# Performance work log

Measured on AMD Instinct MI355X. Metric: run time of the kernel, lower is better.

Reference implementation:

```python
import jax, jax.numpy as jnp
import numpy as np

EMBED_DIM = 1024
NUM_HEADS = 16
HEAD_DIM = EMBED_DIM // NUM_HEADS
MASKED = True


def setup_inputs() -> dict:
    key = jax.random.key(0)
    ks = jax.random.split(key, 9)
    B, S, E = 4, 2048, EMBED_DIM
    sc = 1.0 / np.sqrt(E)
    return {
        "x": jax.random.normal(ks[0], (B, S, E), jnp.float32),
        "wq": jax.random.normal(ks[1], (E, E), jnp.float32) * sc,
        "bq": jax.random.normal(ks[2], (E,), jnp.float32) * 0.02,
        "wk": jax.random.normal(ks[3], (E, E), jnp.float32) * sc,
        "bk": jax.random.normal(ks[4], (E,), jnp.float32) * 0.02,
        "wv": jax.random.normal(ks[5], (E, E), jnp.float32) * sc,
        "bv": jax.random.normal(ks[6], (E,), jnp.float32) * 0.02,
        "wo": jax.random.normal(ks[7], (E, E), jnp.float32) * sc,
        "bo": jax.random.normal(ks[8], (E,), jnp.float32) * 0.02,
    }


def reference(x, wq, bq, wk, bk, wv, bv, wo, bo):
    B, S, E = x.shape
    H, Dh = NUM_HEADS, HEAD_DIM
    # QKV projections, then split heads: [B,S,E] -> [B,H,S,Dh]
    def split(t):
        return t.reshape(B, S, H, Dh).transpose(0, 2, 1, 3)
    q = split(x @ wq.T + bq)
    k = split(x @ wk.T + bk)
    v = split(x @ wv.T + bv)
    scale = Dh ** 0.5
    scores = jnp.einsum('bhsd,bhtd->bhst', q, k) / scale  # [B,H,S,S]
    if MASKED:
        causal = jnp.tril(jnp.ones((S, S), dtype=bool))
        scores = jnp.where(causal, scores, -jnp.inf)
    weights = jax.nn.softmax(scores, axis=-1)
    ctx = jnp.einsum('bhst,bhtd->bhsd', weights, v)
    ctx = ctx.transpose(0, 2, 1, 3).reshape(B, S, E)
    return ctx @ wo.T + bo
```

## Files before the change

kernel.cpp:

```cpp
#include <hip/hip_runtime.h>
#include <hip/hip_bf16.h>

#define EMB   1024
#define SEQ   2048
#define BATCH 4
#define NH    16
#define DHEAD 64
#define MROWS (BATCH*SEQ)
#define NSTRIP (SEQ/32)
#define QSCALE 0.18033688011112042f

typedef float f32x4  __attribute__((ext_vector_type(4)));
typedef float f32x16 __attribute__((ext_vector_type(16)));
typedef short s16x8  __attribute__((ext_vector_type(8)));

__device__ __forceinline__ f32x4 mfma16(s16x8 a, s16x8 b, f32x4 c) {
    return __builtin_amdgcn_mfma_f32_16x16x32_bf16(a, b, c, 0, 0, 0);
}
__device__ __forceinline__ f32x16 mfma32(s16x8 a, s16x8 b, f32x16 c) {
    return __builtin_amdgcn_mfma_f32_32x32x16_bf16(a, b, c, 0, 0, 0);
}

__device__ __forceinline__ unsigned short f2bf(float f) {
    __hip_bfloat16 h = __float2bfloat16(f);
    return __builtin_bit_cast(unsigned short, h);
}

__device__ __forceinline__ unsigned cvtpk(float lo, float hi) {
    unsigned r;
    asm("v_cvt_pk_bf16_f32 %0, %1, %2" : "=v"(r) : "v"(lo), "v"(hi));
    return r;
}

__device__ __forceinline__ void plane_swap(unsigned &a, unsigned &b) {
    asm("v_permlane32_swap_b32 %0, %1" : "+v"(a), "+v"(b));
}

__device__ __forceinline__ s16x8 frag4(unsigned a, unsigned b, unsigned c, unsigned d) {
    union { unsigned u[4]; s16x8 f; } x;
    x.u[0] = a; x.u[1] = b; x.u[2] = c; x.u[3] = d;
    return x.f;
}

__device__ __forceinline__ float exp2r(float x) {
    float r;
    asm("v_exp_f32 %0, %1" : "=v"(r) : "v"(x));
    return r;
}
__device__ __forceinline__ float max3f(float a, float b, float c) {
    float r;
    asm("v_max3_f32 %0, %1, %2, %3" : "=v"(r) : "v"(a), "v"(b), "v"(c));
    return r;
}

__global__ void cvt_all(const float* __restrict__ x,
                        const float* __restrict__ w0, const float* __restrict__ w1,
                        const float* __restrict__ w2, const float* __restrict__ w3,
                        unsigned short* __restrict__ xb,
                        unsigned short* __restrict__ o0, unsigned short* __restrict__ o1,
                        unsigned short* __restrict__ o2, unsigned short* __restrict__ o3,
                        int nx4, int nw4) {
    int i = blockIdx.x * blockDim.x + threadIdx.x;
    const float* in; unsigned short* out; int n;
    switch (blockIdx.y) {
        case 0:  in = x;  out = xb; n = nx4; break;
        case 1:  in = w0; out = o0; n = nw4; break;
        case 2:  in = w1; out = o1; n = nw4; break;
        case 3:  in = w2; out = o2; n = nw4; break;
        default: in = w3; out = o3; n = nw4; break;
    }
    if (i >= n) return;
    float4 v = reinterpret_cast<const float4*>(in)[i];
    ushort4 o;
    o.x = f2bf(v.x); o.y = f2bf(v.y); o.z = f2bf(v.z); o.w = f2bf(v.w);
    reinterpret_cast<ushort4*>(out)[i] = o;
}

#define GLDS(g, s) __builtin_amdgcn_global_load_lds((const __attribute__((address_space(1))) void*)(g), \
                       (__attribute__((address_space(3))) void*)(s), 16, 0, 0)

__global__ __launch_bounds__(256) void gemm_qkv(const unsigned short* __restrict__ A,
                                                const unsigned short* __restrict__ wqb,
                                                const unsigned short* __restrict__ wkb,
                                                const unsigned short* __restrict__ wvb,
                                                const float* __restrict__ bq,
                                                const float* __restrict__ bk,
                                                const float* __restrict__ bv,
                                                unsigned short* __restrict__ qB,
                                                unsigned short* __restrict__ kB,
                                                unsigned short* __restrict__ vtB) {
    __shared__ unsigned short sA0[128*32];
    __shared__ unsigned short sB0[128*32];
    __shared__ unsigned short sA1[128*32];
    __shared__ unsigned short sB1[128*32];
    const int tid = threadIdx.x;
    const int w  = tid >> 6, l = tid & 63;
    const int lg = l >> 4,  lr = l & 15;
    const int nb  = blockIdx.x;
    const int seg = nb >> 3;
    const int mBase = blockIdx.y * 128;
    const int nBase = (nb & 7) * 128;
    const unsigned short* Bw = (seg == 0) ? wqb : (seg == 1) ? wkb : wvb;
    const float* bias = (seg == 0) ? bq : (seg == 1) ? bk : bv;
    const int wr = w >> 1, wc = w & 1;
    const int srow = l >> 2;
    const int sk0  = (l & 3) * 8;
    const bool segV = (seg == 2);

    f32x4 acc[4][4] = {};

    auto STAGE = [&](unsigned short* dA, unsigned short* dB, int kb) {
        #pragma unroll
        for (int rr = 0; rr < 2; ++rr) {
            const int chunk = w + rr * 4;
            const unsigned short* ga = A  + (size_t)(mBase + chunk*16 + srow) * EMB + kb + sk0;
            GLDS(ga, &dA[chunk * 512]);
            const unsigned short* gb = Bw + (size_t)(nBase + chunk*16 + srow) * EMB + kb + sk0;
            GLDS(gb, &dB[chunk * 512]);
        }
    };
    auto COMPUTE = [&](const unsigned short* dA, const unsigned short* dB) {
        s16x8 af[4], bf[4];
        #pragma unroll
        for (int mi = 0; mi < 4; ++mi)
            af[mi] = *reinterpret_cast<const s16x8*>(&dA[(wr*64 + mi*16 + lr)*32 + lg*8]);
        #pragma unroll
        for (int ni = 0; ni < 4; ++ni)
            bf[ni] = *reinterpret_cast<const s16x8*>(&dB[(wc*64 + ni*16 + lr)*32 + lg*8]);
        if (segV) {
            #pragma unroll
            for (int mi = 0; mi < 4; ++mi)
                #pragma unroll
                for (int ni = 0; ni < 4; ++ni)
                    acc[ni][mi] = mfma16(bf[ni], af[mi], acc[ni][mi]);
        } else {
            #pragma unroll
            for (int mi = 0; mi < 4; ++mi)
                #pragma unroll
                for (int ni = 0; ni < 4; ++ni)
                    acc[mi][ni] = mfma16(af[mi], bf[ni], acc[mi][ni]);
        }
    };

    STAGE(sA0, sB0, 0);
    __syncthreads();
    for (int kb = 0; kb < EMB; kb += 64) {
        STAGE(sA1, sB1, kb + 32);
        COMPUTE(sA0, sB0);
        __syncthreads();
        if (kb + 64 < EMB) STAGE(sA0, sB0, kb + 64);
        COMPUTE(sA1, sB1);
        __syncthreads();
    }

    const int colBase = nBase + wc * 64;
    const int rowBase = mBase + wr * 64;
    if (!segV) {
        unsigned short* outp = seg ? kB : qB;
        const float oscale = seg ? 1.0f : QSCALE;
        #pragma unroll
        for (int ni = 0; ni < 4; ++ni) {
            const int col = colBase + ni*16 + lr;
            const float bv = bias[col];
            const int h = col >> 6, d = col & 63;
            const int inner = ((d >> 4) * 2 + ((d >> 3) & 1)) * 256 + (d & 7);
            #pragma unroll
            for (int mi = 0; mi < 4; ++mi) {
                #pragma unroll
                for (int r = 0; r < 4; ++r) {
                    const int gr = rowBase + mi*16 + lg*4 + r;
                    const int b = gr >> 11, sin_ = gr & 2047;
                    const int strip = sin_ >> 5, l31q = sin_ & 31;
                    outp[(size_t)(b*NH + h) * (SEQ*DHEAD) + strip*2048 + inner + l31q*8]
                        = f2bf((acc[mi][ni][r] + bv) * oscale);
                }
            }
        }
    } else {
        #pragma unroll
        for (int ni = 0; ni < 4; ++ni) {
            #pragma unroll
            for (int r = 0; r < 4; ++r) {
                const int n = colBase + ni*16 + lg*4 + r;
                const float bv = bias[n];
                const int h = n >> 6, d = n & 63;
                #pragma unroll
                for (int mi = 0; mi < 4; ++mi) {
                    const int tok = rowBase + mi*16 + lr;
                    const int b = tok >> 11, sv = tok & 2047;
                    const int kvt = sv >> 5, ks = (sv >> 4) & 1, hi2 = (sv >> 3) & 1, j = sv & 7;
                    vtB[(size_t)(b*NH + h) * (SEQ*DHEAD) + kvt*2048 + (ks*2 + hi2)*512 + d*8 + j]
                        = f2bf(acc[ni][mi][r] + bv);
                }
            }
        }
    }
}

__global__ __launch_bounds__(256) void gemm_out(const unsigned short* __restrict__ A,
                                                const unsigned short* __restrict__ Bw,
                                                const float* __restrict__ bias,
                                                float* __restrict__ Out) {
    __shared__ unsigned short sA0[128*32];
    __shared__ unsigned short sB0[128*32];
    __shared__ unsigned short sA1[128*32];
    __shared__ unsigned short sB1[128*32];
    const int tid = threadIdx.x;
    const int w  = tid >> 6, l = tid & 63;
    const int lg = l >> 4,  lr = l & 15;
    const int mBase = blockIdx.y * 128;
    const int nBase = blockIdx.x * 128;
    const int wr = w >> 1, wc = w & 1;
    const int srow = l >> 2;
    const int sk0  = (l & 3) * 8;

    f32x4 acc[4][4] = {};

    auto STAGE = [&](unsigned short* dA, unsigned short* dB, int kb) {
        #pragma unroll
        for (int rr = 0; rr < 2; ++rr) {
            const int chunk = w + rr * 4;
            const unsigned short* ga = A  + (size_t)(mBase + chunk*16 + srow) * EMB + kb + sk0;
            GLDS(ga, &dA[chunk * 512]);
            const unsigned short* gb = Bw + (size_t)(nBase + chunk*16 + srow) * EMB + kb + sk0;
            GLDS(gb, &dB[chunk * 512]);
        }
    };
    auto COMPUTE = [&](const unsigned short* dA, const unsigned short* dB) {
        s16x8 af[4], bf[4];
        #pragma unroll
        for (int mi = 0; mi < 4; ++mi)
            af[mi] = *reinterpret_cast<const s16x8*>(&dA[(wr*64 + mi*16 + lr)*32 + lg*8]);
        #pragma unroll
        for (int ni = 0; ni < 4; ++ni)
            bf[ni] = *reinterpret_cast<const s16x8*>(&dB[(wc*64 + ni*16 + lr)*32 + lg*8]);
        #pragma unroll
        for (int mi = 0; mi < 4; ++mi)
            #pragma unroll
            for (int ni = 0; ni < 4; ++ni)
                acc[mi][ni] = mfma16(af[mi], bf[ni], acc[mi][ni]);
    };

    STAGE(sA0, sB0, 0);
    __syncthreads();
    for (int kb = 0; kb < EMB; kb += 64) {
        STAGE(sA1, sB1, kb + 32);
        COMPUTE(sA0, sB0);
        __syncthreads();
        if (kb + 64 < EMB) STAGE(sA0, sB0, kb + 64);
        COMPUTE(sA1, sB1);
        __syncthreads();
    }

    const int colBase = nBase + wc * 64;
    const int rowBase = mBase + wr * 64;
    #pragma unroll
    for (int ni = 0; ni < 4; ++ni) {
        const int col = colBase + ni*16 + lr;
        const float bv = bias[col];
        #pragma unroll
        for (int mi = 0; mi < 4; ++mi) {
            #pragma unroll
            for (int r = 0; r < 4; ++r) {
                const int gr = rowBase + mi*16 + lg*4 + r;
                Out[(size_t)gr * EMB + col] = acc[mi][ni][r] + bv;
            }
        }
    }
}

__global__ __launch_bounds__(128) void attn_fwd(const unsigned short* __restrict__ qb,
                                                const unsigned short* __restrict__ kb,
                                                const unsigned short* __restrict__ vb,
                                                unsigned short* __restrict__ ctx) {
    __shared__ __align__(16) unsigned sld[2][32*36];
    const int tid = threadIdx.x;
    const int wv_ = tid >> 6;
    const int l = tid & 63;
    const int l31 = l & 31, hi = l >> 5;
    const int bh = blockIdx.x & 63;
    const int pair = (int)blockIdx.x >> 6;
    const int strip = wv_ ? (NSTRIP - 1 - pair) : pair;
    const int q0 = strip * 32;
    const size_t hbase = (size_t)bh * SEQ * DHEAD;
    const unsigned short* qh = qb + hbase;
    const unsigned short* kh = kb + hbase;
    const unsigned short* vh = vb + hbase;

    s16x8 qf[4];
    #pragma unroll
    for (int s = 0; s < 4; ++s)
        qf[s] = *reinterpret_cast<const s16x8*>(&qh[strip*2048 + s*512 + l*8]);

    f32x16 o0 = {}, o1 = {};
    float m = -__builtin_inff(), lsum = 0.f;
    const int ntiles = strip + 1;

    s16x8 kfA[4], vfA[4], kfB[4], vfB[4];

    auto LOADKV = [&](s16x8* kf, s16x8* vf, int t) {
        const unsigned short* kp = kh + t*2048;
        #pragma unroll
        for (int s = 0; s < 4; ++s)
            kf[s] = *reinterpret_cast<const s16x8*>(&kp[s*512 + l*8]);
        const unsigned short* vp = vh + t*2048 + hi*512 + l31*8;
        #pragma unroll
        for (int ks = 0; ks < 2; ++ks) {
            vf[ks]     = *reinterpret_cast<const s16x8*>(&vp[ks*1024]);
            vf[2 + ks] = *reinterpret_cast<const s16x8*>(&vp[ks*1024 + 256]);
        }
    };

    auto BODY = [&](s16x8* kf, s16x8* vf, int t) {
        f32x16 sa = {};
        #pragma unroll
        for (int s = 0; s < 4; ++s) sa = mfma32(kf[s], qf[s], sa);

        if (t == strip) {
            #pragma unroll
            for (int r = 0; r < 16; ++r) {
                const int kvloc = (r & 3) + 8*(r >> 2) + 4*hi;
                if (kvloc > l31) sa[r] = -__builtin_inff();
            }
        }

        const float a0 = max3f(sa[0],  sa[1],  sa[2]);
        const float a1 = max3f(sa[3],  sa[4],  sa[5]);
        const float a2 = max3f(sa[6],  sa[7],  sa[8]);
        const float a3 = max3f(sa[9],  sa[10], sa[11]);
        const float a4 = max3f(sa[12], sa[13], sa[14]);
        const float b0 = max3f(a0, a1, a2);
        const float b1 = max3f(a3, a4, sa[15]);
        float pm = fmaxf(b0, b1);
        pm = fmaxf(pm, __shfl_xor(pm, 32));

        float mn = m;
        if (!__all(pm <= m + 8.0f)) {
            mn = fmaxf(m, pm);
            const float fs = exp2r(m - mn);
            o0 *= fs; o1 *= fs; lsum *= fs;
            m = mn;
        }

        #pragma unroll
        for (int r = 0; r < 16; ++r) sa[r] = exp2r(sa[r] - mn);

        const float s0 = sa[0]+sa[1],   s1 = sa[2]+sa[3],   s2 = sa[4]+sa[5],   s3 = sa[6]+sa[7];
        const float s4 = sa[8]+sa[9],   s5 = sa[10]+sa[11], s6 = sa[12]+sa[13], s7 = sa[14]+sa[15];
        const float t0 = s0+s1, t1 = s2+s3, t2 = s4+s5, t3 = s6+s7;
        float rs = (t0+t1) + (t2+t3);
        rs += __shfl_xor(rs, 32);
        lsum += rs;

        unsigned u[4], v[4];
        #pragma unroll
        for (int r2 = 0; r2 < 4; ++r2) {
            u[r2] = cvtpk(sa[4*r2 + 0], sa[4*r2 + 1]);
            v[r2] = cvtpk(sa[4*r2 + 2], sa[4*r2 + 3]);
        }
        plane_swap(u[0], u[1]); plane_swap(v[0], v[1]);
        plane_swap(u[2], u[3]); plane_swap(v[2], v[3]);
        const s16x8 pf0 = frag4(u[0], v[0], u[1], v[1]);
        const s16x8 pf1 = frag4(u[2], v[2], u[3], v[3]);

        o0 = mfma32(vf[0], pf0, o0);
        o0 = mfma32(vf[1], pf1, o0);
        o1 = mfma32(vf[2], pf0, o1);
        o1 = mfma32(vf[3], pf1, o1);
    };

    LOADKV(kfA, vfA, 0);
    int t = 0;
    for (; t + 1 < ntiles; t += 2) {
        LOADKV(kfB, vfB, t + 1);
        BODY(kfA, vfA, t);
        if (t + 2 < ntiles) LOADKV(kfA, vfA, t + 2);
        BODY(kfB, vfB, t + 1);
    }
    if (t < ntiles) BODY(kfA, vfA, t);

    const float inv = 1.0f / lsum;
    unsigned* my = sld[wv_];
    #pragma unroll
    for (int dt = 0; dt < 2; ++dt) {
        #pragma unroll
        for (int r2 = 0; r2 < 4; ++r2) {
            const float e0 = (dt ? o1[4*r2+0] : o0[4*r2+0]) * inv;
            const float e1 = (dt ? o1[4*r2+1] : o0[4*r2+1]) * inv;
            const float e2 = (dt ? o1[4*r2+2] : o0[4*r2+2]) * inv;
            const float e3 = (dt ? o1[4*r2+3] : o0[4*r2+3]) * inv;
            const int col = 4*r2 + 2*hi + 16*dt;
            my[l31*36 + col]     = cvtpk(e0, e1);
            my[l31*36 + col + 1] = cvtpk(e2, e3);
        }
    }
    asm volatile("s_waitcnt lgkmcnt(0)" ::: "memory");
    __builtin_amdgcn_sched_barrier(0);
    const int row = l >> 1, half = l & 1;
    const unsigned* rp = &my[row*36 + half*16];
    const int b = bh >> 4, h = bh & 15;
    unsigned short* op = &ctx[((size_t)b*SEQ + q0 + row) * EMB + h*DHEAD + half*32];
    #pragma unroll
    for (int i = 0; i < 4; ++i) {
        uint4 d4 = *reinterpret_cast<const uint4*>(rp + i*4);
        *reinterpret_cast<uint4*>(op + i*8) = d4;
    }
}

extern "C" void kernel_launch(void* const* d_in, const int* in_sizes, int n_in,
                              void* d_out, int out_size, void* d_ws, size_t ws_size,
                              hipStream_t stream) {
    const float* x  = (const float*)d_in[0];
    const float* wq = (const float*)d_in[1];
    const float* bq = (const float*)d_in[2];
    const float* wk = (const float*)d_in[3];
    const float* bk = (const float*)d_in[4];
    const float* wv = (const float*)d_in[5];
    const float* bv = (const float*)d_in[6];
    const float* wo = (const float*)d_in[7];
    const float* bo = (const float*)d_in[8];
    float* out = (float*)d_out;

    char* ws = (char*)d_ws;
    const size_t MB = 1ull << 20;
    unsigned short* xb  = (unsigned short*)(ws);
    unsigned short* wqb = (unsigned short*)(ws + 16*MB);
    unsigned short* wkb = (unsigned short*)(ws + 18*MB);
    unsigned short* wvb = (unsigned short*)(ws + 20*MB);
    unsigned short* wob = (unsigned short*)(ws + 22*MB);
    unsigned short* qB  = (unsigned short*)(ws + 24*MB);
    unsigned short* kB  = (unsigned short*)(ws + 40*MB);
    unsigned short* vtB = (unsigned short*)(ws + 56*MB);
    unsigned short* ctx = xb;

    const int nx4 = MROWS * EMB / 4;
    const int nw4 = EMB * EMB / 4;
    cvt_all<<<dim3((nx4 + 255)/256, 5), 256, 0, stream>>>(x, wq, wk, wv, wo,
                                                          xb, wqb, wkb, wvb, wob, nx4, nw4);

    gemm_qkv<<<dim3(24, MROWS/128), 256, 0, stream>>>(xb, wqb, wkb, wvb, bq, bk, bv, qB, kB, vtB);

    attn_fwd<<<dim3((NSTRIP/2) * BATCH * NH), 128, 0, stream>>>(qB, kB, vtB, ctx);

    gemm_out<<<dim3(EMB/128, MROWS/128), 256, 0, stream>>>(ctx, wob, bo, out);
}
```

Before: 191.9 us.

## Process both paired query strips in one wave sharing K/V loads

The attention kernel moves from two waves per block, each handling one of a pair of causal query strips, to a single wave that handles both strips. Each K/V tile is loaded once and applied to both the low and high strip, which halves K/V global traffic for the shared tiles. The cost is doubled accumulator and Q-fragment register pressure, which may lower occupancy. It also leaves half as many waves in flight, with each wave running the longer serial tile loop.

Measured after the change: 215.3 us. 1.12x slower.

```diff
diff --git a/kernel.cpp b/kernel.cpp
--- a/kernel.cpp
+++ b/kernel.cpp
@@ -269,32 +269,32 @@
     }
 }
 
-__global__ __launch_bounds__(128) void attn_fwd(const unsigned short* __restrict__ qb,
-                                                const unsigned short* __restrict__ kb,
-                                                const unsigned short* __restrict__ vb,
-                                                unsigned short* __restrict__ ctx) {
+__global__ __launch_bounds__(64) void attn_fwd(const unsigned short* __restrict__ qb,
+                                               const unsigned short* __restrict__ kb,
+                                               const unsigned short* __restrict__ vb,
+                                               unsigned short* __restrict__ ctx) {
     __shared__ __align__(16) unsigned sld[2][32*36];
-    const int tid = threadIdx.x;
-    const int wv_ = tid >> 6;
-    const int l = tid & 63;
+    const int l = threadIdx.x;
     const int l31 = l & 31, hi = l >> 5;
     const int bh = blockIdx.x & 63;
     const int pair = (int)blockIdx.x >> 6;
-    const int strip = wv_ ? (NSTRIP - 1 - pair) : pair;
-    const int q0 = strip * 32;
+    const int sL = pair, sH = NSTRIP - 1 - pair;
     const size_t hbase = (size_t)bh * SEQ * DHEAD;
     const unsigned short* qh = qb + hbase;
     const unsigned short* kh = kb + hbase;
     const unsigned short* vh = vb + hbase;
 
-    s16x8 qf[4];
+    s16x8 qfL[4], qfH[4];
     #pragma unroll
-    for (int s = 0; s < 4; ++s)
-        qf[s] = *reinterpret_cast<const s16x8*>(&qh[strip*2048 + s*512 + l*8]);
-
-    f32x16 o0 = {}, o1 = {};
-    float m = -__builtin_inff(), lsum = 0.f;
-    const int ntiles = strip + 1;
+    for (int s = 0; s < 4; ++s) {
+        qfL[s] = *reinterpret_cast<const s16x8*>(&qh[sL*2048 + s*512 + l*8]);
+        qfH[s] = *reinterpret_cast<const s16x8*>(&qh[sH*2048 + s*512 + l*8]);
+    }
+
+    f32x16 oL0 = {}, oL1 = {}, oH0 = {}, oH1 = {};
+    float mL = -__builtin_inff(), lsL = 0.f;
+    float mH = -__builtin_inff(), lsH = 0.f;
+    const int ntiles = sH + 1;
 
     s16x8 kfA[4], vfA[4], kfB[4], vfB[4];
 
@@ -311,7 +311,8 @@
         }
     };
 
-    auto BODY = [&](s16x8* kf, s16x8* vf, int t) {
+    auto BODY = [&](const s16x8* kf, const s16x8* vf, const s16x8* qf,
+                    f32x16& o0, f32x16& o1, float& m, float& lsum, int t, int strip) {
         f32x16 sa = {};
         #pragma unroll
         for (int s = 0; s < 4; ++s) sa = mfma32(kf[s], qf[s], sa);
@@ -369,42 +370,50 @@
         o1 = mfma32(vf[3], pf1, o1);
     };
 
+    auto STEP = [&](const s16x8* kf, const s16x8* vf, int t) {
+        if (t <= sL) BODY(kf, vf, qfL, oL0, oL1, mL, lsL, t, sL);
+        BODY(kf, vf, qfH, oH0, oH1, mH, lsH, t, sH);
+    };
+
     LOADKV(kfA, vfA, 0);
     int t = 0;
     for (; t + 1 < ntiles; t += 2) {
         LOADKV(kfB, vfB, t + 1);
-        BODY(kfA, vfA, t);
+        STEP(kfA, vfA, t);
         if (t + 2 < ntiles) LOADKV(kfA, vfA, t + 2);
-        BODY(kfB, vfB, t + 1);
-    }
-    if (t < ntiles) BODY(kfA, vfA, t);
-
-    const float inv = 1.0f / lsum;
-    unsigned* my = sld[wv_];
-    #pragma unroll
-    for (int dt = 0; dt < 2; ++dt) {
-        #pragma unroll
-        for (int r2 = 0; r2 < 4; ++r2) {
-            const float e0 = (dt ? o1[4*r2+0] : o0[4*r2+0]) * inv;
-            const float e1 = (dt ? o1[4*r2+1] : o0[4*r2+1]) * inv;
-            const float e2 = (dt ? o1[4*r2+2] : o0[4*r2+2]) * inv;
-            const float e3 = (dt ? o1[4*r2+3] : o0[4*r2+3]) * inv;
-            const int col = 4*r2 + 2*hi + 16*dt;
-            my[l31*36 + col]     = cvtpk(e0, e1);
-            my[l31*36 + col + 1] = cvtpk(e2, e3);
-        }
-    }
-    asm volatile("s_waitcnt lgkmcnt(0)" ::: "memory");
-    __builtin_amdgcn_sched_barrier(0);
-    const int row = l >> 1, half = l & 1;
-    const unsigned* rp = &my[row*36 + half*16];
+        STEP(kfB, vfB, t + 1);
+    }
+    if (t < ntiles) STEP(kfA, vfA, t);
+
     const int b = bh >> 4, h = bh & 15;
-    unsigned short* op = &ctx[((size_t)b*SEQ + q0 + row) * EMB + h*DHEAD + half*32];
-    #pragma unroll
-    for (int i = 0; i < 4; ++i) {
-        uint4 d4 = *reinterpret_cast<const uint4*>(rp + i*4);
-        *reinterpret_cast<uint4*>(op + i*8) = d4;
-    }
+    auto EPI = [&](const f32x16& o0, const f32x16& o1, float lsum, int strip, unsigned* my) {
+        const float inv = 1.0f / lsum;
+        #pragma unroll
+        for (int dt = 0; dt < 2; ++dt) {
+            #pragma unroll
+            for (int r2 = 0; r2 < 4; ++r2) {
+                const float e0 = (dt ? o1[4*r2+0] : o0[4*r2+0]) * inv;
+                const float e1 = (dt ? o1[4*r2+1] : o0[4*r2+1]) * inv;
+                const float e2 = (dt ? o1[4*r2+2] : o0[4*r2+2]) * inv;
+                const float e3 = (dt ? o1[4*r2+3] : o0[4*r2+3]) * inv;
+                const int col = 4*r2 + 2*hi + 16*dt;
+                my[l31*36 + col]     = cvtpk(e0, e1);
+                my[l31*36 + col + 1] = cvtpk(e2, e3);
+            }
+        }
+        asm volatile("s_waitcnt lgkmcnt(0)" ::: "memory");
+        __builtin_amdgcn_sched_barrier(0);
+        const int row = l >> 1, half = l & 1;
+        const unsigned* rp = &my[row*36 + half*16];
+        unsigned short* op = &ctx[((size_t)b*SEQ + strip*32 + row) * EMB + h*DHEAD + half*32];
+        #pragma unroll
+        for (int i = 0; i < 4; ++i) {
+            uint4 d4 = *reinterpret_cast<const uint4*>(rp + i*4);
+            *reinterpret_cast<uint4*>(op + i*8) = d4;
+        }
+    };
+    EPI(oL0, oL1, lsL, sL, sld[0]);
+    EPI(oH0, oH1, lsH, sH, sld[1]);
 }
 
 extern "C" void kernel_launch(void* const* d_in, const int* in_sizes, int n_in,
@@ -440,7 +449,7 @@
 
     gemm_qkv<<<dim3(24, MROWS/128), 256, 0, stream>>>(xb, wqb, wkb, wvb, bq, bk, bv, qB, kB, vtB);
 
-    attn_fwd<<<dim3((NSTRIP/2) * BATCH * NH), 128, 0, stream>>>(qB, kB, vtB, ctx);
+    attn_fwd<<<dim3((NSTRIP/2) * BATCH * NH), 64, 0, stream>>>(qB, kB, vtB, ctx);
 
     gemm_out<<<dim3(EMB/128, MROWS/128), 256, 0, stream>>>(ctx, wob, bo, out);
 }
```

## Triple-buffer GEMM LDS staging and split attention into one-wave blocks

Applied to the files above, without the earlier changes.

Both GEMM kernels move from a double-buffered loop with two full __syncthreads per 64-K step to a three-buffer rotating ring. Each 32-K step waits on vmcnt for only the oldest stage and issues one barrier, which keeps two global-to-LDS loads in flight. The attention kernel changes from 128-thread blocks that pair a short and a long causal strip to 64-thread single-wave blocks, one strip each. Longest strips are launched first for load balance. This gives up the explicit pairing in exchange for more, smaller blocks and uses more LDS per GEMM block.

After: 199.5 us. 3.9% more time.

```diff
diff --git a/kernel.cpp b/kernel.cpp
--- a/kernel.cpp
+++ b/kernel.cpp
@@ -78,6 +78,7 @@
 
 #define GLDS(g, s) __builtin_amdgcn_global_load_lds((const __attribute__((address_space(1))) void*)(g), \
                        (__attribute__((address_space(3))) void*)(s), 16, 0, 0)
+#define MEMF asm volatile("" ::: "memory")
 
 __global__ __launch_bounds__(256) void gemm_qkv(const unsigned short* __restrict__ A,
                                                 const unsigned short* __restrict__ wqb,
@@ -89,10 +90,8 @@
                                                 unsigned short* __restrict__ qB,
                                                 unsigned short* __restrict__ kB,
                                                 unsigned short* __restrict__ vtB) {
-    __shared__ unsigned short sA0[128*32];
-    __shared__ unsigned short sB0[128*32];
-    __shared__ unsigned short sA1[128*32];
-    __shared__ unsigned short sB1[128*32];
+    __shared__ unsigned short sA0[128*32], sA1[128*32], sA2[128*32];
+    __shared__ unsigned short sB0[128*32], sB1[128*32], sB2[128*32];
     const int tid = threadIdx.x;
     const int w  = tid >> 6, l = tid & 63;
     const int lg = l >> 4,  lr = l & 15;
@@ -142,15 +141,22 @@
         }
     };
 
-    STAGE(sA0, sB0, 0);
-    __syncthreads();
-    for (int kb = 0; kb < EMB; kb += 64) {
-        STAGE(sA1, sB1, kb + 32);
-        COMPUTE(sA0, sB0);
-        __syncthreads();
-        if (kb + 64 < EMB) STAGE(sA0, sB0, kb + 64);
-        COMPUTE(sA1, sB1);
-        __syncthreads();
+    unsigned short *a0 = sA0, *a1 = sA1, *a2 = sA2;
+    unsigned short *b0 = sB0, *b1 = sB1, *b2 = sB2;
+    STAGE(a0, b0, 0);
+    STAGE(a1, b1, 32);
+    MEMF;
+    for (int kb = 0; kb < EMB; kb += 32) {
+        if (kb + 32 < EMB) { asm volatile("s_waitcnt vmcnt(4)" ::: "memory"); }
+        else               { asm volatile("s_waitcnt vmcnt(0)" ::: "memory"); }
+        __builtin_amdgcn_s_barrier();
+        MEMF;
+        if (kb + 64 < EMB) STAGE(a2, b2, kb + 64);
+        COMPUTE(a0, b0);
+        MEMF;
+        unsigned short* t_;
+        t_ = a0; a0 = a1; a1 = a2; a2 = t_;
+        t_ = b0; b0 = b1; b1 = b2; b2 = t_;
     }
 
     const int colBase = nBase + wc * 64;
@@ -201,10 +207,8 @@
                                                 const unsigned short* __restrict__ Bw,
                                                 const float* __restrict__ bias,
                                                 float* __restrict__ Out) {
-    __shared__ unsigned short sA0[128*32];
-    __shared__ unsigned short sB0[128*32];
-    __shared__ unsigned short sA1[128*32];
-    __shared__ unsigned short sB1[128*32];
+    __shared__ unsigned short sA0[128*32], sA1[128*32], sA2[128*32];
+    __shared__ unsigned short sB0[128*32], sB1[128*32], sB2[128*32];
     const int tid = threadIdx.x;
     const int w  = tid >> 6, l = tid & 63;
     const int lg = l >> 4,  lr = l & 15;
@@ -241,15 +245,22 @@
                 acc[mi][ni] = mfma16(af[mi], bf[ni], acc[mi][ni]);
     };
 
-    STAGE(sA0, sB0, 0);
-    __syncthreads();
-    for (int kb = 0; kb < EMB; kb += 64) {
-        STAGE(sA1, sB1, kb + 32);
-        COMPUTE(sA0, sB0);
-        __syncthreads();
-        if (kb + 64 < EMB) STAGE(sA0, sB0, kb + 64);
-        COMPUTE(sA1, sB1);
-        __syncthreads();
+    unsigned short *a0 = sA0, *a1 = sA1, *a2 = sA2;
+    unsigned short *b0 = sB0, *b1 = sB1, *b2 = sB2;
+    STAGE(a0, b0, 0);
+    STAGE(a1, b1, 32);
+    MEMF;
+    for (int kb = 0; kb < EMB; kb += 32) {
+        if (kb + 32 < EMB) { asm volatile("s_waitcnt vmcnt(4)" ::: "memory"); }
+        else               { asm volatile("s_waitcnt vmcnt(0)" ::: "memory"); }
+        __builtin_amdgcn_s_barrier();
+        MEMF;
+        if (kb + 64 < EMB) STAGE(a2, b2, kb + 64);
+        COMPUTE(a0, b0);
+        MEMF;
+        unsigned short* t_;
+        t_ = a0; a0 = a1; a1 = a2; a2 = t_;
+        t_ = b0; b0 = b1; b1 = b2; b2 = t_;
     }
 
     const int colBase = nBase + wc * 64;
@@ -269,18 +280,15 @@
     }
 }
 
-__global__ __launch_bounds__(128) void attn_fwd(const unsigned short* __restrict__ qb,
-                                                const unsigned short* __restrict__ kb,
-                                                const unsigned short* __restrict__ vb,
-                                                unsigned short* __restrict__ ctx) {
-    __shared__ __align__(16) unsigned sld[2][32*36];
-    const int tid = threadIdx.x;
-    const int wv_ = tid >> 6;
-    const int l = tid & 63;
+__global__ __launch_bounds__(64) void attn_fwd(const unsigned short* __restrict__ qb,
+                                               const unsigned short* __restrict__ kb,
+                                               const unsigned short* __restrict__ vb,
+                                               unsigned short* __restrict__ ctx) {
+    __shared__ __align__(16) unsigned sld[32*36];
+    const int l = threadIdx.x;
     const int l31 = l & 31, hi = l >> 5;
     const int bh = blockIdx.x & 63;
-    const int pair = (int)blockIdx.x >> 6;
-    const int strip = wv_ ? (NSTRIP - 1 - pair) : pair;
+    const int strip = (NSTRIP - 1) - ((int)blockIdx.x >> 6);
     const int q0 = strip * 32;
     const size_t hbase = (size_t)bh * SEQ * DHEAD;
     const unsigned short* qh = qb + hbase;
@@ -380,7 +388,6 @@
     if (t < ntiles) BODY(kfA, vfA, t);
 
     const float inv = 1.0f / lsum;
-    unsigned* my = sld[wv_];
     #pragma unroll
     for (int dt = 0; dt < 2; ++dt) {
         #pragma unroll
@@ -390,14 +397,14 @@
             const float e2 = (dt ? o1[4*r2+2] : o0[4*r2+2]) * inv;
             const float e3 = (dt ? o1[4*r2+3] : o0[4*r2+3]) * inv;
             const int col = 4*r2 + 2*hi + 16*dt;
-            my[l31*36 + col]     = cvtpk(e0, e1);
-            my[l31*36 + col + 1] = cvtpk(e2, e3);
+            sld[l31*36 + col]     = cvtpk(e0, e1);
+            sld[l31*36 + col + 1] = cvtpk(e2, e3);
         }
     }
     asm volatile("s_waitcnt lgkmcnt(0)" ::: "memory");
     __builtin_amdgcn_sched_barrier(0);
     const int row = l >> 1, half = l & 1;
-    const unsigned* rp = &my[row*36 + half*16];
+    const unsigned* rp = &sld[row*36 + half*16];
     const int b = bh >> 4, h = bh & 15;
     unsigned short* op = &ctx[((size_t)b*SEQ + q0 + row) * EMB + h*DHEAD + half*32];
     #pragma unroll
@@ -440,7 +447,7 @@
 
     gemm_qkv<<<dim3(24, MROWS/128), 256, 0, stream>>>(xb, wqb, wkb, wvb, bq, bk, bv, qB, kB, vtB);
 
-    attn_fwd<<<dim3((NSTRIP/2) * BATCH * NH), 128, 0, stream>>>(qB, kB, vtB, ctx);
+    attn_fwd<<<dim3(NSTRIP * BATCH * NH), 64, 0, stream>>>(qB, kB, vtB, ctx);
 
     gemm_out<<<dim3(EMB/128, MROWS/128), 256, 0, stream>>>(ctx, wob, bo, out);
 }
```
